# Performance work log

Measured on AMD Instinct MI355X. Metric: run time of the kernel, lower is better.

Reference implementation:

```python
import jax, jax.numpy as jnp
import numpy as np

GROUP = 64          # quantization group size (axis=0 grouping)
IN_F = 4096
OUT_F = 11008
N_GROUPS = IN_F * OUT_F // GROUP  # 704512


def setup_inputs() -> dict:
    key = jax.random.key(0)
    k0, k1, k2, k3, k4 = jax.random.split(key, 5)
    x = jax.random.normal(k0, (4, 2048, IN_F), dtype=jnp.float32)
    # packed 4-bit codes: two codes per byte, rows 0..31 hold high nibbles,
    # unpacked rows 32..63 come from low nibbles (HQQ pack_4bit_u8 layout)
    W_q = jax.random.randint(k1, (GROUP // 2, N_GROUPS), 0, 256, dtype=jnp.int32)
    # scale here is meta['scale'] = 1/quant_scale, i.e. the dequant multiplier
    scale = jax.random.uniform(k2, (1, N_GROUPS), dtype=jnp.float32) * 0.01 + 1e-4
    zero = jax.random.uniform(k3, (1, N_GROUPS), dtype=jnp.float32) * 15.0
    bias = jax.random.normal(k4, (OUT_F,), dtype=jnp.float32) * 0.01
    return {"x": x, "W_q": W_q, "scale": scale, "zero": zero, "bias": bias}


def _dequantize(W_q, scale, zero):
    # unpack_4bit_u8: high nibble -> first half of rows, low nibble -> second half
    high = (W_q >> 4) & 0xF
    low = W_q & 0xF
    W_r = jnp.concatenate([high, low], axis=0).astype(jnp.float32)  # [64, N_GROUPS]
    W = (W_r - zero) * scale                                        # affine dequant
    return W.reshape(OUT_F, IN_F)


def reference(x, W_q, scale, zero, bias):
    W = _dequantize(W_q, scale, zero)          # [out, in]
    out = jnp.einsum('bsi,oi->bso', x, W)      # x @ W.T
    return out + bias
```

## Files before the change

kernel.cpp:

```cpp
#include <hip/hip_runtime.h>


#define K_DIM 4096
#define N_DIM 11008
#define M_DIM 8192
#define NG 704512

#define BM 256
#define BN 256
#define BK 64
#define NKT 64
#define NIT 32

typedef __bf16 bf16;
typedef bf16 bf16x4 __attribute__((ext_vector_type(4)));
typedef bf16 bf16x8 __attribute__((ext_vector_type(8)));
typedef float f32x4 __attribute__((ext_vector_type(4)));

__device__ __forceinline__ void async_copy16(const void* g, void* l) {
  __builtin_amdgcn_global_load_lds(
      (const __attribute__((address_space(1))) void*)g,
      (__attribute__((address_space(3))) void*)l,
      16, 0, 0);
}

__device__ __forceinline__ void barrier_() {
  asm volatile("" ::: "memory");
  __builtin_amdgcn_s_barrier();
  asm volatile("" ::: "memory");
}
#define VMW(n) asm volatile("s_waitcnt vmcnt(" #n ")" ::: "memory")

__global__ void cvt_x(const float* __restrict__ X, bf16* __restrict__ Xb) {
  const int idx = (blockIdx.x * 256 + threadIdx.x) * 4;
  const float4 v = *(const float4*)(X + idx);
  bf16x4 o;
  o[0] = (bf16)v.x; o[1] = (bf16)v.y; o[2] = (bf16)v.z; o[3] = (bf16)v.w;
  *(bf16x4*)(Xb + idx) = o;
}

__global__ void dequant_w(const int* __restrict__ Wq, const float* __restrict__ scale,
                          const float* __restrict__ zero, bf16* __restrict__ Wb) {
  const int idx = blockIdx.x * 256 + threadIdx.x;
  const int r = idx / (NG / 4);
  const int g = (idx - r * (NG / 4)) * 4;
  const int4 q = *(const int4*)(Wq + r * NG + g);
  const float4 sc = *(const float4*)(scale + g);
  const float4 zp = *(const float4*)(zero + g);
  const int c = g >> 12;
  const int i = g & 4095;
  bf16x4 hi, lo;
  hi[0] = (bf16)(((float)((q.x >> 4) & 0xF) - zp.x) * sc.x);
  hi[1] = (bf16)(((float)((q.y >> 4) & 0xF) - zp.y) * sc.y);
  hi[2] = (bf16)(((float)((q.z >> 4) & 0xF) - zp.z) * sc.z);
  hi[3] = (bf16)(((float)((q.w >> 4) & 0xF) - zp.w) * sc.w);
  lo[0] = (bf16)(((float)(q.x & 0xF) - zp.x) * sc.x);
  lo[1] = (bf16)(((float)(q.y & 0xF) - zp.y) * sc.y);
  lo[2] = (bf16)(((float)(q.z & 0xF) - zp.z) * sc.z);
  lo[3] = (bf16)(((float)(q.w & 0xF) - zp.w) * sc.w);
  *(bf16x4*)(Wb + (size_t)(r * 172 + c) * 4096 + i) = hi;
  *(bf16x4*)(Wb + (size_t)((r + 32) * 172 + c) * 4096 + i) = lo;
}

__global__ __launch_bounds__(512, 2)
void gemm_bt(const bf16* __restrict__ A, const bf16* __restrict__ B,
             const float* __restrict__ bias, float* __restrict__ C) {
  extern __shared__ char smem[];

  const int tid = threadIdx.x;
  const int wave = tid >> 6;
  const int lane = tid & 63;
  const int l15 = lane & 15;
  const int quad = lane >> 4;
  const int wm = wave >> 2;
  const int wn = wave & 3;

  const int id = blockIdx.x;
  const int wg = (id & 7) * 172 + (id >> 3);
  const int bm = (wg & 31) * BM;
  const int bn = (wg >> 5) * BN;

  const int srow = tid >> 3;
  const int qc = (tid & 7) ^ (srow & 7);
  const bf16* sA = A + (size_t)(bm + srow) * K_DIM + qc * 8;
  const bf16* sB = B + (size_t)(bn + srow) * K_DIM + qc * 8;
  const int ldsWave = wave << 10;

  auto stageA = [&](int b, int h, int t) {
    const bf16* g = sA + (size_t)(h * 128) * K_DIM + (size_t)t * BK;
    char* l = smem + (b * 2 + h) * 16384 + ldsWave;
    async_copy16(g, l);
    async_copy16(g + (size_t)64 * K_DIM, l + 8192);
  };
  auto stageB = [&](int b, int h, int t) {
    const bf16* g = sB + (size_t)(h * 128) * K_DIM + (size_t)t * BK;
    char* l = smem + 65536 + (b * 2 + h) * 16384 + ldsWave;
    async_copy16(g, l);
    async_copy16(g + (size_t)64 * K_DIM, l + 8192);
  };

  const int sw = l15 & 7;
  const int ro = l15 * 128;
  const int k0 = (quad ^ sw) << 4;
  const int k1 = ((quad + 4) ^ sw) << 4;
  const char* rdA0 = smem + wm * 16384 + ro;
  const char* rdB0 = smem + 65536 + (wn >> 1) * 16384 + (wn & 1) * 8192 + ro;
  const char* rdA1 = rdA0 + 32768;
  const char* rdB1 = rdB0 + 32768;

  auto ldA = [&](bf16x8 (&d)[4][2], const char* base, int fm) {
#pragma unroll
    for (int m = 0; m < 4; ++m) {
      const char* p = base + (fm + m) * 2048;
      d[m][0] = *(const bf16x8*)(p + k0);
      d[m][1] = *(const bf16x8*)(p + k1);
    }
  };
  auto ldB = [&](bf16x8 (&d)[2][2], const char* base, int gn) {
#pragma unroll
    for (int n = 0; n < 2; ++n) {
      const char* p = base + (gn + n) * 2048;
      d[n][0] = *(const bf16x8*)(p + k0);
      d[n][1] = *(const bf16x8*)(p + k1);
    }
  };

  f32x4 acc[8][4];
#pragma unroll
  for (int m = 0; m < 8; ++m)
#pragma unroll
    for (int n = 0; n < 4; ++n) {
      f32x4 z = {0.f, 0.f, 0.f, 0.f};
      acc[m][n] = z;
    }

  auto mmq = [&](bf16x8 (&a)[4][2], bf16x8 (&b)[2][2], int fm, int gn) {
    __builtin_amdgcn_s_setprio(1);
#pragma unroll
    for (int m = 0; m < 4; ++m)
#pragma unroll
      for (int n = 0; n < 2; ++n) {
        acc[fm + m][gn + n] = __builtin_amdgcn_mfma_f32_16x16x32_bf16(
            a[m][0], b[n][0], acc[fm + m][gn + n], 0, 0, 0);
        acc[fm + m][gn + n] = __builtin_amdgcn_mfma_f32_16x16x32_bf16(
            a[m][1], b[n][1], acc[fm + m][gn + n], 0, 0, 0);
      }
    __builtin_amdgcn_s_setprio(0);
    __builtin_amdgcn_sched_barrier(0);
  };

  bf16x8 a0[4][2], a1[4][2], p0[2][2], p1[2][2];

  stageB(0, 0, 0); stageB(0, 1, 0); stageA(0, 0, 0); stageA(0, 1, 0);
  stageB(1, 0, 1); stageB(1, 1, 1);
  VMW(4);
  barrier_();
  ldA(a0, rdA0, 0); ldB(p0, rdB0, 0);

  for (int it = 0; it < NIT; ++it) {
    const int t1 = 2 * it + 1, t2 = 2 * it + 2, t3 = 2 * it + 3;
    const bool more = (it < NIT - 1);

    stageA(1, 0, t1);
    barrier_();
    ldB(p1, rdB0, 2);
    mmq(a0, p0, 0, 0);
    barrier_();
    stageA(1, 1, t1);
    barrier_();
    ldA(a1, rdA0, 4);
    mmq(a0, p1, 0, 2);
    barrier_();
    if (more) stageB(0, 0, t2);
    barrier_();
    mmq(a1, p0, 4, 0);
    barrier_();
    if (more) { stageB(0, 1, t2); VMW(4); } else { VMW(0); }
    barrier_();
    ldA(a0, rdA1, 0); ldB(p0, rdB1, 0);
    mmq(a1, p1, 4, 2);
    barrier_();
    if (more) stageA(0, 0, t2);
    barrier_();
    ldB(p1, rdB1, 2);
    mmq(a0, p0, 0, 0);
    barrier_();
    if (more) stageA(0, 1, t2);
    barrier_();
    ldA(a1, rdA1, 4);
    mmq(a0, p1, 0, 2);
    barrier_();
    if (more) stageB(1, 0, t3);
    barrier_();
    mmq(a1, p0, 4, 0);
    barrier_();
    if (more) { stageB(1, 1, t3); VMW(4); }
    barrier_();
    if (more) { ldA(a0, rdA0, 0); ldB(p0, rdB0, 0); }
    mmq(a1, p1, 4, 2);
    barrier_();
  }

  const int cm = bm + wm * 128 + quad * 4;
  const int cn = bn + wn * 64 + l15;
#pragma unroll
  for (int g = 0; g < 4; ++g) {
    const int col = cn + g * 16;
    const float bv = bias[col];
#pragma unroll
    for (int m = 0; m < 8; ++m) {
      float* cp = C + (size_t)(cm + m * 16) * N_DIM + col;
      const f32x4 a = acc[m][g];
      __builtin_nontemporal_store(a[0] + bv, cp + 0 * N_DIM);
      __builtin_nontemporal_store(a[1] + bv, cp + 1 * N_DIM);
      __builtin_nontemporal_store(a[2] + bv, cp + 2 * N_DIM);
      __builtin_nontemporal_store(a[3] + bv, cp + 3 * N_DIM);
    }
  }
}

extern "C" void kernel_launch(void* const* d_in, const int* in_sizes, int n_in,
                              void* d_out, int out_size, void* d_ws, size_t ws_size,
                              hipStream_t stream) {
  const float* x = (const float*)d_in[0];
  const int* Wq = (const int*)d_in[1];
  const float* scale = (const float*)d_in[2];
  const float* zero = (const float*)d_in[3];
  const float* bias = (const float*)d_in[4];
  float* out = (float*)d_out;

  bf16* Xb = (bf16*)d_ws;
  bf16* Wb = (bf16*)((char*)d_ws + (size_t)67108864);

  static int smem_set = 0;
  if (!smem_set) {
    (void)hipFuncSetAttribute((const void*)gemm_bt,
                              hipFuncAttributeMaxDynamicSharedMemorySize, 131072);
    smem_set = 1;
  }

  cvt_x<<<32768, 256, 0, stream>>>(x, Xb);
  dequant_w<<<22016, 256, 0, stream>>>(Wq, scale, zero, Wb);
  gemm_bt<<<1376, 512, 131072, stream>>>(Xb, Wb, bias, out);
}
```

Before: 1.070 ms.

## Restructure GEMM main loop into K-split MFMA phases with pointer-advancing staging

Rewrites the GEMM inner schedule: each phase now issues 16 MFMAs over a full 4x4 subtile at one K-half, instead of 8 MFMAs over 4x2 subtiles covering both K-halves. It also halves the number of barriers per iteration, stages A and B together using incrementing pointers and XOR double-buffer toggling, and peels the last iteration so the loop needs no conditionals. Separately, the cvt_x and dequant_w prepass kernels are widened to process 8 elements per thread with 16-byte stores. The risks are the full vmcnt(0) waits and a changed overlap between LDS reads and async copies.

Result: slower. 1.114 ms (+4.2%).

```diff
diff --git a/kernel.cpp b/kernel.cpp
--- a/kernel.cpp
+++ b/kernel.cpp
@@ -9,7 +9,6 @@
 #define BM 256
 #define BN 256
 #define BK 64
-#define NKT 64
 #define NIT 32
 
 typedef __bf16 bf16;
@@ -32,34 +31,47 @@
 #define VMW(n) asm volatile("s_waitcnt vmcnt(" #n ")" ::: "memory")
 
 __global__ void cvt_x(const float* __restrict__ X, bf16* __restrict__ Xb) {
-  const int idx = (blockIdx.x * 256 + threadIdx.x) * 4;
-  const float4 v = *(const float4*)(X + idx);
-  bf16x4 o;
-  o[0] = (bf16)v.x; o[1] = (bf16)v.y; o[2] = (bf16)v.z; o[3] = (bf16)v.w;
-  *(bf16x4*)(Xb + idx) = o;
+  const int idx = (blockIdx.x * 256 + threadIdx.x) * 8;
+  const float4 v0 = *(const float4*)(X + idx);
+  const float4 v1 = *(const float4*)(X + idx + 4);
+  bf16x8 o;
+  o[0] = (bf16)v0.x; o[1] = (bf16)v0.y; o[2] = (bf16)v0.z; o[3] = (bf16)v0.w;
+  o[4] = (bf16)v1.x; o[5] = (bf16)v1.y; o[6] = (bf16)v1.z; o[7] = (bf16)v1.w;
+  *(bf16x8*)(Xb + idx) = o;
 }
 
 __global__ void dequant_w(const int* __restrict__ Wq, const float* __restrict__ scale,
                           const float* __restrict__ zero, bf16* __restrict__ Wb) {
   const int idx = blockIdx.x * 256 + threadIdx.x;
-  const int r = idx / (NG / 4);
-  const int g = (idx - r * (NG / 4)) * 4;
-  const int4 q = *(const int4*)(Wq + r * NG + g);
-  const float4 sc = *(const float4*)(scale + g);
-  const float4 zp = *(const float4*)(zero + g);
+  const int r = idx / (NG / 8);
+  const int g = (idx - r * (NG / 8)) * 8;
+  const int4 q0 = *(const int4*)(Wq + (size_t)r * NG + g);
+  const int4 q1 = *(const int4*)(Wq + (size_t)r * NG + g + 4);
+  const float4 sc0 = *(const float4*)(scale + g);
+  const float4 sc1 = *(const float4*)(scale + g + 4);
+  const float4 zp0 = *(const float4*)(zero + g);
+  const float4 zp1 = *(const float4*)(zero + g + 4);
   const int c = g >> 12;
   const int i = g & 4095;
-  bf16x4 hi, lo;
-  hi[0] = (bf16)(((float)((q.x >> 4) & 0xF) - zp.x) * sc.x);
-  hi[1] = (bf16)(((float)((q.y >> 4) & 0xF) - zp.y) * sc.y);
-  hi[2] = (bf16)(((float)((q.z >> 4) & 0xF) - zp.z) * sc.z);
-  hi[3] = (bf16)(((float)((q.w >> 4) & 0xF) - zp.w) * sc.w);
-  lo[0] = (bf16)(((float)(q.x & 0xF) - zp.x) * sc.x);
-  lo[1] = (bf16)(((float)(q.y & 0xF) - zp.y) * sc.y);
-  lo[2] = (bf16)(((float)(q.z & 0xF) - zp.z) * sc.z);
-  lo[3] = (bf16)(((float)(q.w & 0xF) - zp.w) * sc.w);
-  *(bf16x4*)(Wb + (size_t)(r * 172 + c) * 4096 + i) = hi;
-  *(bf16x4*)(Wb + (size_t)((r + 32) * 172 + c) * 4096 + i) = lo;
+  bf16x8 hi, lo;
+  hi[0] = (bf16)(((float)((q0.x >> 4) & 0xF) - zp0.x) * sc0.x);
+  hi[1] = (bf16)(((float)((q0.y >> 4) & 0xF) - zp0.y) * sc0.y);
+  hi[2] = (bf16)(((float)((q0.z >> 4) & 0xF) - zp0.z) * sc0.z);
+  hi[3] = (bf16)(((float)((q0.w >> 4) & 0xF) - zp0.w) * sc0.w);
+  hi[4] = (bf16)(((float)((q1.x >> 4) & 0xF) - zp1.x) * sc1.x);
+  hi[5] = (bf16)(((float)((q1.y >> 4) & 0xF) - zp1.y) * sc1.y);
+  hi[6] = (bf16)(((float)((q1.z >> 4) & 0xF) - zp1.z) * sc1.z);
+  hi[7] = (bf16)(((float)((q1.w >> 4) & 0xF) - zp1.w) * sc1.w);
+  lo[0] = (bf16)(((float)(q0.x & 0xF) - zp0.x) * sc0.x);
+  lo[1] = (bf16)(((float)(q0.y & 0xF) - zp0.y) * sc0.y);
+  lo[2] = (bf16)(((float)(q0.z & 0xF) - zp0.z) * sc0.z);
+  lo[3] = (bf16)(((float)(q0.w & 0xF) - zp0.w) * sc0.w);
+  lo[4] = (bf16)(((float)(q1.x & 0xF) - zp1.x) * sc1.x);
+  lo[5] = (bf16)(((float)(q1.y & 0xF) - zp1.y) * sc1.y);
+  lo[6] = (bf16)(((float)(q1.z & 0xF) - zp1.z) * sc1.z);
+  lo[7] = (bf16)(((float)(q1.w & 0xF) - zp1.w) * sc1.w);
+  *(bf16x8*)(Wb + (size_t)(r * 172 + c) * 4096 + i) = hi;
+  *(bf16x8*)(Wb + (size_t)((r + 32) * 172 + c) * 4096 + i) = lo;
 }
 
 __global__ __launch_bounds__(512, 2)
@@ -82,21 +94,22 @@
 
   const int srow = tid >> 3;
   const int qc = (tid & 7) ^ (srow & 7);
-  const bf16* sA = A + (size_t)(bm + srow) * K_DIM + qc * 8;
-  const bf16* sB = B + (size_t)(bn + srow) * K_DIM + qc * 8;
   const int ldsWave = wave << 10;
 
-  auto stageA = [&](int b, int h, int t) {
-    const bf16* g = sA + (size_t)(h * 128) * K_DIM + (size_t)t * BK;
-    char* l = smem + (b * 2 + h) * 16384 + ldsWave;
-    async_copy16(g, l);
-    async_copy16(g + (size_t)64 * K_DIM, l + 8192);
-  };
-  auto stageB = [&](int b, int h, int t) {
-    const bf16* g = sB + (size_t)(h * 128) * K_DIM + (size_t)t * BK;
-    char* l = smem + 65536 + (b * 2 + h) * 16384 + ldsWave;
-    async_copy16(g, l);
-    async_copy16(g + (size_t)64 * K_DIM, l + 8192);
+  const bf16* pA0 = A + (size_t)(bm + srow) * K_DIM + qc * 8;
+  const bf16* pA1 = pA0 + (size_t)128 * K_DIM;
+  const bf16* pB0 = B + (size_t)(bn + srow) * K_DIM + qc * 8;
+  const bf16* pB1 = pB0 + (size_t)128 * K_DIM;
+  char* lA0 = smem + 0 + ldsWave;
+  char* lA1 = smem + 16384 + ldsWave;
+  char* lB0 = smem + 65536 + ldsWave;
+  char* lB1 = smem + 65536 + 16384 + ldsWave;
+
+  auto stage = [&](const bf16*& gp, char*& lp) {
+    async_copy16(gp, lp);
+    async_copy16(gp + (size_t)64 * K_DIM, lp + 8192);
+    gp += BK;
+    lp = (char*)((unsigned long long)lp ^ 32768ull);
   };
 
   const int sw = l15 & 7;
@@ -108,21 +121,15 @@
   const char* rdA1 = rdA0 + 32768;
   const char* rdB1 = rdB0 + 32768;
 
-  auto ldA = [&](bf16x8 (&d)[4][2], const char* base, int fm) {
-#pragma unroll
-    for (int m = 0; m < 4; ++m) {
-      const char* p = base + (fm + m) * 2048;
-      d[m][0] = *(const bf16x8*)(p + k0);
-      d[m][1] = *(const bf16x8*)(p + k1);
-    }
-  };
-  auto ldB = [&](bf16x8 (&d)[2][2], const char* base, int gn) {
-#pragma unroll
-    for (int n = 0; n < 2; ++n) {
-      const char* p = base + (gn + n) * 2048;
-      d[n][0] = *(const bf16x8*)(p + k0);
-      d[n][1] = *(const bf16x8*)(p + k1);
-    }
+  auto ldA4 = [&](bf16x8 (&d)[4], const char* base, int fm, int kb) {
+#pragma unroll
+    for (int m = 0; m < 4; ++m)
+      d[m] = *(const bf16x8*)(base + (fm + m) * 2048 + kb);
+  };
+  auto ldB4 = [&](bf16x8 (&d)[4], const char* base, int kb) {
+#pragma unroll
+    for (int n = 0; n < 4; ++n)
+      d[n] = *(const bf16x8*)(base + n * 2048 + kb);
   };
 
   f32x4 acc[8][4];
@@ -134,72 +141,84 @@
       acc[m][n] = z;
     }
 
-  auto mmq = [&](bf16x8 (&a)[4][2], bf16x8 (&b)[2][2], int fm, int gn) {
+  auto mmq = [&](bf16x8 (&a)[4], bf16x8 (&b)[4], int mh) {
     __builtin_amdgcn_s_setprio(1);
 #pragma unroll
     for (int m = 0; m < 4; ++m)
 #pragma unroll
-      for (int n = 0; n < 2; ++n) {
-        acc[fm + m][gn + n] = __builtin_amdgcn_mfma_f32_16x16x32_bf16(
-            a[m][0], b[n][0], acc[fm + m][gn + n], 0, 0, 0);
-        acc[fm + m][gn + n] = __builtin_amdgcn_mfma_f32_16x16x32_bf16(
-            a[m][1], b[n][1], acc[fm + m][gn + n], 0, 0, 0);
-      }
+      for (int n = 0; n < 4; ++n)
+        acc[mh + m][n] = __builtin_amdgcn_mfma_f32_16x16x32_bf16(
+            a[m], b[n], acc[mh + m][n], 0, 0, 0);
     __builtin_amdgcn_s_setprio(0);
     __builtin_amdgcn_sched_barrier(0);
   };
 
-  bf16x8 a0[4][2], a1[4][2], p0[2][2], p1[2][2];
-
-  stageB(0, 0, 0); stageB(0, 1, 0); stageA(0, 0, 0); stageA(0, 1, 0);
-  stageB(1, 0, 1); stageB(1, 1, 1);
+  bf16x8 aA[4], aB[4], bP[4], bQ[4];
+
+  stage(pA0, lA0); stage(pA1, lA1); stage(pB0, lB0); stage(pB1, lB1);
+  stage(pB0, lB0); stage(pB1, lB1);
   VMW(4);
   barrier_();
-  ldA(a0, rdA0, 0); ldB(p0, rdB0, 0);
-
-  for (int it = 0; it < NIT; ++it) {
-    const int t1 = 2 * it + 1, t2 = 2 * it + 2, t3 = 2 * it + 3;
-    const bool more = (it < NIT - 1);
-
-    stageA(1, 0, t1);
-    barrier_();
-    ldB(p1, rdB0, 2);
-    mmq(a0, p0, 0, 0);
-    barrier_();
-    stageA(1, 1, t1);
-    barrier_();
-    ldA(a1, rdA0, 4);
-    mmq(a0, p1, 0, 2);
-    barrier_();
-    if (more) stageB(0, 0, t2);
-    barrier_();
-    mmq(a1, p0, 4, 0);
-    barrier_();
-    if (more) { stageB(0, 1, t2); VMW(4); } else { VMW(0); }
-    barrier_();
-    ldA(a0, rdA1, 0); ldB(p0, rdB1, 0);
-    mmq(a1, p1, 4, 2);
-    barrier_();
-    if (more) stageA(0, 0, t2);
-    barrier_();
-    ldB(p1, rdB1, 2);
-    mmq(a0, p0, 0, 0);
-    barrier_();
-    if (more) stageA(0, 1, t2);
-    barrier_();
-    ldA(a1, rdA1, 4);
-    mmq(a0, p1, 0, 2);
-    barrier_();
-    if (more) stageB(1, 0, t3);
-    barrier_();
-    mmq(a1, p0, 4, 0);
-    barrier_();
-    if (more) { stageB(1, 1, t3); VMW(4); }
-    barrier_();
-    if (more) { ldA(a0, rdA0, 0); ldB(p0, rdB0, 0); }
-    mmq(a1, p1, 4, 2);
-    barrier_();
+  ldA4(aA, rdA0, 0, k0); ldB4(bP, rdB0, k0);
+
+  for (int it = 0; it < NIT - 1; ++it) {
+    barrier_();
+    ldA4(aB, rdA0, 4, k0); ldB4(bQ, rdB0, k1);
+    stage(pA0, lA0); stage(pA1, lA1);
+    mmq(aA, bP, 0);
+    barrier_();
+    ldA4(aA, rdA0, 0, k1);
+    mmq(aB, bP, 4);
+    barrier_();
+    ldA4(aB, rdA0, 4, k1);
+    mmq(aA, bQ, 0);
+    VMW(0);
+    barrier_();
+    ldA4(aA, rdA1, 0, k0); ldB4(bP, rdB1, k0);
+    stage(pB0, lB0); stage(pB1, lB1);
+    mmq(aB, bQ, 4);
+    barrier_();
+    ldA4(aB, rdA1, 4, k0); ldB4(bQ, rdB1, k1);
+    stage(pA0, lA0); stage(pA1, lA1);
+    mmq(aA, bP, 0);
+    barrier_();
+    ldA4(aA, rdA1, 0, k1);
+    mmq(aB, bP, 4);
+    barrier_();
+    ldA4(aB, rdA1, 4, k1);
+    mmq(aA, bQ, 0);
+    VMW(0);
+    barrier_();
+    ldA4(aA, rdA0, 0, k0); ldB4(bP, rdB0, k0);
+    stage(pB0, lB0); stage(pB1, lB1);
+    mmq(aB, bQ, 4);
   }
+
+  barrier_();
+  ldA4(aB, rdA0, 4, k0); ldB4(bQ, rdB0, k1);
+  stage(pA0, lA0); stage(pA1, lA1);
+  mmq(aA, bP, 0);
+  barrier_();
+  ldA4(aA, rdA0, 0, k1);
+  mmq(aB, bP, 4);
+  barrier_();
+  ldA4(aB, rdA0, 4, k1);
+  mmq(aA, bQ, 0);
+  VMW(0);
+  barrier_();
+  ldA4(aA, rdA1, 0, k0); ldB4(bP, rdB1, k0);
+  mmq(aB, bQ, 4);
+  barrier_();
+  ldA4(aB, rdA1, 4, k0); ldB4(bQ, rdB1, k1);
+  mmq(aA, bP, 0);
+  barrier_();
+  ldA4(aA, rdA1, 0, k1);
+  mmq(aB, bP, 4);
+  barrier_();
+  ldA4(aB, rdA1, 4, k1);
+  mmq(aA, bQ, 0);
+  barrier_();
+  mmq(aB, bQ, 4);
 
   const int cm = bm + wm * 128 + quad * 4;
   const int cn = bn + wn * 64 + l15;
@@ -239,7 +258,7 @@
     smem_set = 1;
   }
 
-  cvt_x<<<32768, 256, 0, stream>>>(x, Xb);
-  dequant_w<<<22016, 256, 0, stream>>>(Wq, scale, zero, Wb);
+  cvt_x<<<16384, 256, 0, stream>>>(x, Xb);
+  dequant_w<<<11008, 256, 0, stream>>>(Wq, scale, zero, Wb);
   gemm_bt<<<1376, 512, 131072, stream>>>(Xb, Wb, bias, out);
 }
```
